# Kernel optimization log

Measured on AMD Instinct MI355X. Metric: run time of the kernel, lower is better.

The kernel has to match this reference:

```python
import jax, jax.numpy as jnp
import numpy as np

N_NODES = 10000
N_EDGES = 320000


def _graph_conv(x, W, b, src, dst, n):
    # DGL GraphConv, norm='both': D_out^{-1/2} on src side, aggregate, D_in^{-1/2} on dst side,
    # then linear + bias. Degrees clamped at 1 (allow_zero_in_degree=True).
    ones = jnp.ones(src.shape[0], dtype=x.dtype)
    deg_out = jnp.clip(jax.ops.segment_sum(ones, src, num_segments=n), 1.0)
    deg_in = jnp.clip(jax.ops.segment_sum(ones, dst, num_segments=n), 1.0)
    h = x * jax.lax.rsqrt(deg_out)[:, None]          # [n, f] scaled source feats
    agg = jax.ops.segment_sum(h[src], dst, num_segments=n)  # gather + scatter-add
    agg = agg * jax.lax.rsqrt(deg_in)[:, None]
    return agg @ W + b


def setup_inputs() -> dict:
    key = jax.random.key(0)
    ks = jax.random.split(key, 8)
    in_dim, h1, h2 = 512, 256, 128
    features = jax.random.normal(ks[0], (N_NODES, in_dim), dtype=jnp.float32)
    src = jax.random.randint(ks[1], (N_EDGES,), 0, N_NODES)
    dst = jax.random.randint(ks[2], (N_EDGES,), 0, N_NODES)
    noise = jax.random.normal(ks[3], (N_NODES, h2), dtype=jnp.float32)
    W1 = jax.random.normal(ks[4], (in_dim, h1), dtype=jnp.float32) / np.sqrt(in_dim)
    b1 = jnp.zeros((h1,), dtype=jnp.float32)
    W2 = jax.random.normal(ks[5], (h1, h2), dtype=jnp.float32) / np.sqrt(h1)
    b2 = jnp.zeros((h2,), dtype=jnp.float32)
    W3 = jax.random.normal(ks[6], (h1, h2), dtype=jnp.float32) / np.sqrt(h1)
    b3 = jnp.zeros((h2,), dtype=jnp.float32)
    return {"features": features, "src": src, "dst": dst, "noise": noise,
            "W1": W1, "b1": b1, "W2": W2, "b2": b2, "W3": W3, "b3": b3}


def reference(features, src, dst, noise, W1, b1, W2, b2, W3, b3):
    n = features.shape[0]
    h = jax.nn.relu(_graph_conv(features, W1, b1, src, dst, n))
    mean = _graph_conv(h, W2, b2, src, dst, n)
    log_std = _graph_conv(h, W3, b3, src, dst, n)
    z = mean + noise * jnp.exp(log_std)              # reparameterization
    adj_rec = jax.nn.sigmoid(z @ z.T)                # inner-product decoder [N, N]
    return adj_rec
```

## Files before the change

kernel.cpp:

```cpp
#include <hip/hip_runtime.h>
#include <hip/hip_fp16.h>


#define NN 10000
#define NE 320000
#define FD 512
#define H1 256
#define H2 128

typedef _Float16 half8 __attribute__((ext_vector_type(8)));
typedef _Float16 half4 __attribute__((ext_vector_type(4)));
typedef float f32x4 __attribute__((ext_vector_type(4)));

__global__ void k_zero3(int* __restrict__ a, int* __restrict__ b, int* __restrict__ c, int n) {
    int i = blockIdx.x * blockDim.x + threadIdx.x;
    if (i < n) { a[i] = 0; b[i] = 0; c[i] = 0; }
}

__global__ void k_count(const int* __restrict__ src, const int* __restrict__ dst,
                        int* __restrict__ co, int* __restrict__ ci) {
    int e = blockIdx.x * blockDim.x + threadIdx.x;
    if (e < NE) {
        atomicAdd(&co[src[e]], 1);
        atomicAdd(&ci[dst[e]], 1);
    }
}

__global__ __launch_bounds__(1024) void k_scan(const int* __restrict__ ci, const int* __restrict__ co,
                                               int* __restrict__ row_ptr,
                                               float* __restrict__ rs_in, float* __restrict__ rs_out) {
    __shared__ int sm[1024];
    int tid = threadIdx.x;
    const int CH = (NN + 1023) / 1024;
    int base = tid * CH;
    int local[CH];
    int s = 0;
    #pragma unroll
    for (int i = 0; i < CH; ++i) {
        int idx = base + i;
        local[i] = s;
        if (idx < NN) s += ci[idx];
    }
    sm[tid] = s;
    __syncthreads();
    for (int off = 1; off < 1024; off <<= 1) {
        int v = (tid >= off) ? sm[tid - off] : 0;
        __syncthreads();
        sm[tid] += v;
        __syncthreads();
    }
    int excl = sm[tid] - s;
    #pragma unroll
    for (int i = 0; i < CH; ++i) {
        int idx = base + i;
        if (idx < NN) row_ptr[idx] = excl + local[i];
    }
    if (tid == 1023) row_ptr[NN] = sm[1023];
    for (int i = tid; i < NN; i += 1024) {
        int a = ci[i], b = co[i];
        rs_in[i]  = rsqrtf((float)(a > 1 ? a : 1));
        rs_out[i] = rsqrtf((float)(b > 1 ? b : 1));
    }
}

__global__ void k_bucket(const int* __restrict__ src, const int* __restrict__ dst,
                         const int* __restrict__ row_ptr, int* __restrict__ cursor,
                         int* __restrict__ esrc) {
    int e = blockIdx.x * blockDim.x + threadIdx.x;
    if (e < NE) {
        int d = dst[e];
        int p = row_ptr[d] + atomicAdd(&cursor[d], 1);
        esrc[p] = src[e];
    }
}

__global__ void k_castW(const float* __restrict__ W1, const float* __restrict__ W2,
                        const float* __restrict__ W3,
                        _Float16* __restrict__ W1Th, _Float16* __restrict__ W1Tl,
                        _Float16* __restrict__ WcTh, _Float16* __restrict__ WcTl) {
    int idx = blockIdx.x * blockDim.x + threadIdx.x;
    if (idx < FD * H1) {
        int k = idx >> 8, n = idx & 255;
        float v = W1[idx];
        _Float16 h = (_Float16)v;
        W1Th[n * FD + k] = h;
        W1Tl[n * FD + k] = (_Float16)(v - (float)h);
    } else if (idx < FD * H1 + H1 * H1) {
        int j = idx - FD * H1;
        int k = j >> 8, n = j & 255;
        float v = (n < H2) ? W2[k * H2 + n] : W3[k * H2 + (n - H2)];
        _Float16 h = (_Float16)v;
        WcTh[n * H1 + k] = h;
        WcTl[n * H1 + k] = (_Float16)(v - (float)h);
    }
}

__global__ __launch_bounds__(256) void k_gemm1(
    const float* __restrict__ A, const float* __restrict__ ascale,
    const _Float16* __restrict__ BTh, const _Float16* __restrict__ BTl,
    _Float16* __restrict__ C, int M) {
    const int K = FD;
    __shared__ __align__(16) _Float16 Ahs[64][72];
    __shared__ __align__(16) _Float16 Als[64][72];
    __shared__ __align__(16) _Float16 Bhs[64][72];
    __shared__ __align__(16) _Float16 Bls[64][72];
    int tid = threadIdx.x;
    int lane = tid & 63;
    int w = tid >> 6;
    int wr = (w >> 1) * 32, wc = (w & 1) * 32;
    int bm = blockIdx.x * 64, bn = blockIdx.y * 64;
    f32x4 acc[2][2] = {};
    for (int k0 = 0; k0 < K; k0 += 64) {
        __syncthreads();
        #pragma unroll
        for (int i = 0; i < 4; ++i) {
            int lin = i * 256 + tid;
            int r = lin >> 4, c = lin & 15;
            int gr = bm + r;
            float4 v = {0.f, 0.f, 0.f, 0.f};
            float s = 1.0f;
            if (gr < M) {
                v = *(const float4*)(A + (size_t)gr * K + k0 + c * 4);
                s = ascale[gr];
            }
            v.x *= s; v.y *= s; v.z *= s; v.w *= s;
            half4 hh = { (_Float16)v.x, (_Float16)v.y, (_Float16)v.z, (_Float16)v.w };
            half4 ll = { (_Float16)(v.x - (float)hh[0]), (_Float16)(v.y - (float)hh[1]),
                         (_Float16)(v.z - (float)hh[2]), (_Float16)(v.w - (float)hh[3]) };
            *(half4*)&Ahs[r][c * 4] = hh;
            *(half4*)&Als[r][c * 4] = ll;
        }
        #pragma unroll
        for (int i = 0; i < 2; ++i) {
            int lin = i * 256 + tid;
            int r = lin >> 3, c = lin & 7;
            *(int4*)&Bhs[r][c * 8] = *(const int4*)(BTh + (size_t)(bn + r) * K + k0 + c * 8);
            *(int4*)&Bls[r][c * 8] = *(const int4*)(BTl + (size_t)(bn + r) * K + k0 + c * 8);
        }
        __syncthreads();
        #pragma unroll
        for (int ks = 0; ks < 2; ++ks) {
            int kof = ks * 32 + ((lane >> 4) << 3);
            half8 ah[2], al[2], bh[2], bl[2];
            #pragma unroll
            for (int f = 0; f < 2; ++f) {
                ah[f] = *(const half8*)&Ahs[wr + f * 16 + (lane & 15)][kof];
                al[f] = *(const half8*)&Als[wr + f * 16 + (lane & 15)][kof];
                bh[f] = *(const half8*)&Bhs[wc + f * 16 + (lane & 15)][kof];
                bl[f] = *(const half8*)&Bls[wc + f * 16 + (lane & 15)][kof];
            }
            #pragma unroll
            for (int i = 0; i < 2; ++i)
                #pragma unroll
                for (int j = 0; j < 2; ++j) {
                    acc[i][j] = __builtin_amdgcn_mfma_f32_16x16x32_f16(ah[i], bh[j], acc[i][j], 0, 0, 0);
                    acc[i][j] = __builtin_amdgcn_mfma_f32_16x16x32_f16(ah[i], bl[j], acc[i][j], 0, 0, 0);
                    acc[i][j] = __builtin_amdgcn_mfma_f32_16x16x32_f16(al[i], bh[j], acc[i][j], 0, 0, 0);
                }
        }
    }
    int quad = lane >> 4, c16 = lane & 15;
    #pragma unroll
    for (int i = 0; i < 2; ++i) {
        int row0 = bm + wr + i * 16 + quad * 4;
        #pragma unroll
        for (int j = 0; j < 2; ++j) {
            int col = bn + wc + j * 16 + c16;
            #pragma unroll
            for (int r = 0; r < 4; ++r) {
                int row = row0 + r;
                if (row < M) C[(size_t)row * H1 + col] = (_Float16)acc[i][j][r];
            }
        }
    }
}

__global__ __launch_bounds__(256) void k_gemm2z(
    const float* __restrict__ A,
    const _Float16* __restrict__ BTh, const _Float16* __restrict__ BTl,
    const float* __restrict__ b2, const float* __restrict__ b3,
    const float* __restrict__ noise, _Float16* __restrict__ Zh, int M) {
    const int K = H1;
    __shared__ __align__(16) _Float16 Ahs[64][72];
    __shared__ __align__(16) _Float16 Als[64][72];
    __shared__ __align__(16) _Float16 Bmh[64][72];
    __shared__ __align__(16) _Float16 Bml[64][72];
    __shared__ __align__(16) _Float16 Blh[64][72];
    __shared__ __align__(16) _Float16 Bll[64][72];
    int tid = threadIdx.x;
    int lane = tid & 63;
    int w = tid >> 6;
    int wr = (w >> 1) * 32, wc = (w & 1) * 32;
    int bm = blockIdx.x * 64;
    int c0 = blockIdx.y * 64;
    f32x4 accm[2][2] = {};
    f32x4 accl[2][2] = {};
    for (int k0 = 0; k0 < K; k0 += 64) {
        __syncthreads();
        #pragma unroll
        for (int i = 0; i < 4; ++i) {
            int lin = i * 256 + tid;
            int r = lin >> 4, c = lin & 15;
            int gr = bm + r;
            float4 v = {0.f, 0.f, 0.f, 0.f};
            if (gr < M) v = *(const float4*)(A + (size_t)gr * K + k0 + c * 4);
            half4 hh = { (_Float16)v.x, (_Float16)v.y, (_Float16)v.z, (_Float16)v.w };
            half4 ll = { (_Float16)(v.x - (float)hh[0]), (_Float16)(v.y - (float)hh[1]),
                         (_Float16)(v.z - (float)hh[2]), (_Float16)(v.w - (float)hh[3]) };
            *(half4*)&Ahs[r][c * 4] = hh;
            *(half4*)&Als[r][c * 4] = ll;
        }
        #pragma unroll
        for (int i = 0; i < 2; ++i) {
            int lin = i * 256 + tid;
            int r = lin >> 3, c = lin & 7;
            size_t rm = (size_t)(c0 + r) * K + k0 + c * 8;
            size_t rl = (size_t)(128 + c0 + r) * K + k0 + c * 8;
            *(int4*)&Bmh[r][c * 8] = *(const int4*)(BTh + rm);
            *(int4*)&Bml[r][c * 8] = *(const int4*)(BTl + rm);
            *(int4*)&Blh[r][c * 8] = *(const int4*)(BTh + rl);
            *(int4*)&Bll[r][c * 8] = *(const int4*)(BTl + rl);
        }
        __syncthreads();
        #pragma unroll
        for (int ks = 0; ks < 2; ++ks) {
            int kof = ks * 32 + ((lane >> 4) << 3);
            half8 ah[2], al[2], mh[2], ml[2], lh[2], ll[2];
            #pragma unroll
            for (int f = 0; f < 2; ++f) {
                ah[f] = *(const half8*)&Ahs[wr + f * 16 + (lane & 15)][kof];
                al[f] = *(const half8*)&Als[wr + f * 16 + (lane & 15)][kof];
                mh[f] = *(const half8*)&Bmh[wc + f * 16 + (lane & 15)][kof];
                ml[f] = *(const half8*)&Bml[wc + f * 16 + (lane & 15)][kof];
                lh[f] = *(const half8*)&Blh[wc + f * 16 + (lane & 15)][kof];
                ll[f] = *(const half8*)&Bll[wc + f * 16 + (lane & 15)][kof];
            }
            #pragma unroll
            for (int i = 0; i < 2; ++i)
                #pragma unroll
                for (int j = 0; j < 2; ++j) {
                    accm[i][j] = __builtin_amdgcn_mfma_f32_16x16x32_f16(ah[i], mh[j], accm[i][j], 0, 0, 0);
                    accm[i][j] = __builtin_amdgcn_mfma_f32_16x16x32_f16(ah[i], ml[j], accm[i][j], 0, 0, 0);
                    accm[i][j] = __builtin_amdgcn_mfma_f32_16x16x32_f16(al[i], mh[j], accm[i][j], 0, 0, 0);
                    accl[i][j] = __builtin_amdgcn_mfma_f32_16x16x32_f16(ah[i], lh[j], accl[i][j], 0, 0, 0);
                    accl[i][j] = __builtin_amdgcn_mfma_f32_16x16x32_f16(ah[i], ll[j], accl[i][j], 0, 0, 0);
                    accl[i][j] = __builtin_amdgcn_mfma_f32_16x16x32_f16(al[i], lh[j], accl[i][j], 0, 0, 0);
                }
        }
    }
    int quad = lane >> 4, c16 = lane & 15;
    #pragma unroll
    for (int i = 0; i < 2; ++i) {
        int row0 = bm + wr + i * 16 + quad * 4;
        #pragma unroll
        for (int j = 0; j < 2; ++j) {
            int c = c0 + wc + j * 16 + c16;
            float bm_ = b2[c], bl_ = b3[c];
            #pragma unroll
            for (int r = 0; r < 4; ++r) {
                int row = row0 + r;
                if (row < M) {
                    float mean = accm[i][j][r] + bm_;
                    float lsv  = accl[i][j][r] + bl_;
                    float z = mean + noise[(size_t)row * H2 + c] * __expf(lsv);
                    Zh[(size_t)row * H2 + c] = (_Float16)z;
                }
            }
        }
    }
}

template <bool FIRST>
__global__ __launch_bounds__(256) void k_agg(const _Float16* __restrict__ in,
                                             _Float16* __restrict__ outh, float* __restrict__ outf,
                                             const int* __restrict__ esrc, const int* __restrict__ row_ptr,
                                             const float* __restrict__ rs_in, const float* __restrict__ rs_out,
                                             const float* __restrict__ bias) {
    int node = (blockIdx.x * blockDim.x + threadIdx.x) >> 6;
    int lane = threadIdx.x & 63;
    if (node >= NN) return;
    int beg = row_ptr[node], end = row_ptr[node + 1];
    float a0 = 0.f, a1 = 0.f, a2 = 0.f, a3 = 0.f;
    int e = beg;
    for (; e + 4 <= end; e += 4) {
        int s0 = esrc[e + 0], s1 = esrc[e + 1], s2 = esrc[e + 2], s3 = esrc[e + 3];
        half4 v0 = ((const half4*)(in + (size_t)s0 * H1))[lane];
        half4 v1 = ((const half4*)(in + (size_t)s1 * H1))[lane];
        half4 v2 = ((const half4*)(in + (size_t)s2 * H1))[lane];
        half4 v3 = ((const half4*)(in + (size_t)s3 * H1))[lane];
        a0 += (float)v0[0] + (float)v1[0] + (float)v2[0] + (float)v3[0];
        a1 += (float)v0[1] + (float)v1[1] + (float)v2[1] + (float)v3[1];
        a2 += (float)v0[2] + (float)v1[2] + (float)v2[2] + (float)v3[2];
        a3 += (float)v0[3] + (float)v1[3] + (float)v2[3] + (float)v3[3];
    }
    for (; e < end; ++e) {
        half4 v0 = ((const half4*)(in + (size_t)esrc[e] * H1))[lane];
        a0 += (float)v0[0]; a1 += (float)v0[1]; a2 += (float)v0[2]; a3 += (float)v0[3];
    }
    float si = rs_in[node];
    a0 *= si; a1 *= si; a2 *= si; a3 *= si;
    if (FIRST) {
        float4 bb = ((const float4*)bias)[lane];
        float so = rs_out[node];
        a0 = fmaxf(a0 + bb.x, 0.f) * so;
        a1 = fmaxf(a1 + bb.y, 0.f) * so;
        a2 = fmaxf(a2 + bb.z, 0.f) * so;
        a3 = fmaxf(a3 + bb.w, 0.f) * so;
        half4 hh = { (_Float16)a0, (_Float16)a1, (_Float16)a2, (_Float16)a3 };
        ((half4*)(outh + (size_t)node * H1))[lane] = hh;
    } else {
        float4 r = { a0, a1, a2, a3 };
        ((float4*)(outf + (size_t)node * H1))[lane] = r;
    }
}

__global__ __launch_bounds__(256) void k_decoder(const _Float16* __restrict__ Z, float* __restrict__ out) {
    __shared__ __align__(16) _Float16 As[128][72];
    __shared__ __align__(16) _Float16 Bs[128][72];
    int tid = threadIdx.x;
    int lane = tid & 63;
    int w = tid >> 6;
    int wrow = (w >> 1) * 64;
    int wcol = (w & 1) * 64;
    int rowBase = blockIdx.y * 128;
    int colBase = blockIdx.x * 128;
    f32x4 acc[4][4] = {};
    for (int s = 0; s < 2; ++s) {
        __syncthreads();
        #pragma unroll
        for (int i = 0; i < 4; ++i) {
            int lin = i * 256 + tid;
            int r = lin >> 3, c = lin & 7;
            int4 v = {0, 0, 0, 0};
            int gr = rowBase + r;
            if (gr < NN) v = *(const int4*)(Z + (size_t)gr * H2 + s * 64 + c * 8);
            *(int4*)&As[r][c * 8] = v;
            int4 u = {0, 0, 0, 0};
            int gc = colBase + r;
            if (gc < NN) u = *(const int4*)(Z + (size_t)gc * H2 + s * 64 + c * 8);
            *(int4*)&Bs[r][c * 8] = u;
        }
        __syncthreads();
        #pragma unroll
        for (int kk = 0; kk < 2; ++kk) {
            int kof = kk * 32 + ((lane >> 4) << 3);
            half8 a[4], b[4];
            #pragma unroll
            for (int f = 0; f < 4; ++f) a[f] = *(const half8*)&As[wrow + f * 16 + (lane & 15)][kof];
            #pragma unroll
            for (int f = 0; f < 4; ++f) b[f] = *(const half8*)&Bs[wcol + f * 16 + (lane & 15)][kof];
            #pragma unroll
            for (int i = 0; i < 4; ++i)
                #pragma unroll
                for (int j = 0; j < 4; ++j)
                    acc[i][j] = __builtin_amdgcn_mfma_f32_16x16x32_f16(a[i], b[j], acc[i][j], 0, 0, 0);
        }
    }
    #pragma unroll
    for (int i = 0; i < 4; ++i) {
        int row0 = rowBase + wrow + i * 16 + ((lane >> 4) << 2);
        #pragma unroll
        for (int j = 0; j < 4; ++j) {
            int col = colBase + wcol + j * 16 + (lane & 15);
            if (col < NN) {
                #pragma unroll
                for (int r = 0; r < 4; ++r) {
                    int row = row0 + r;
                    if (row < NN) {
                        float x = acc[i][j][r];
                        float sg = __builtin_amdgcn_rcpf(1.0f + __expf(-x));
                        __builtin_nontemporal_store(sg, out + (size_t)row * NN + col);
                    }
                }
            }
        }
    }
}

extern "C" void kernel_launch(void* const* d_in, const int* in_sizes, int n_in,
                              void* d_out, int out_size, void* d_ws, size_t ws_size,
                              hipStream_t stream) {
    const float* features = (const float*)d_in[0];
    const int*   src      = (const int*)d_in[1];
    const int*   dst      = (const int*)d_in[2];
    const float* noise    = (const float*)d_in[3];
    const float* W1 = (const float*)d_in[4];
    const float* b1 = (const float*)d_in[5];
    const float* W2 = (const float*)d_in[6];
    const float* b2 = (const float*)d_in[7];
    const float* W3 = (const float*)d_in[8];
    const float* b3 = (const float*)d_in[9];
    float* out = (float*)d_out;
    (void)in_sizes; (void)n_in; (void)out_size; (void)ws_size;

    char* ws = (char*)d_ws;
    size_t off = 0;
    auto alloc = [&](size_t bytes) -> void* {
        void* p = ws + off;
        off += (bytes + 255) & ~(size_t)255;
        return p;
    };
    int* degc_out = (int*)alloc(NN * sizeof(int));
    int* degc_in  = (int*)alloc(NN * sizeof(int));
    int* row_ptr  = (int*)alloc((NN + 1) * sizeof(int));
    int* cursor   = (int*)alloc(NN * sizeof(int));
    int* esrc     = (int*)alloc(NE * sizeof(int));
    float* rs_out = (float*)alloc(NN * sizeof(float));
    float* rs_in  = (float*)alloc(NN * sizeof(float));
    _Float16* W1Th = (_Float16*)alloc((size_t)H1 * FD * sizeof(_Float16));
    _Float16* W1Tl = (_Float16*)alloc((size_t)H1 * FD * sizeof(_Float16));
    _Float16* WcTh = (_Float16*)alloc((size_t)H1 * H1 * sizeof(_Float16));
    _Float16* WcTl = (_Float16*)alloc((size_t)H1 * H1 * sizeof(_Float16));
    _Float16* y1h  = (_Float16*)alloc((size_t)NN * H1 * sizeof(_Float16));
    _Float16* hh   = (_Float16*)alloc((size_t)NN * H1 * sizeof(_Float16));
    float* agg2    = (float*)alloc((size_t)NN * H1 * sizeof(float));
    _Float16* Zh   = (_Float16*)alloc((size_t)NN * H2 * sizeof(_Float16));

    k_zero3<<<(NN + 255) / 256, 256, 0, stream>>>(degc_out, degc_in, cursor, NN);
    k_count<<<(NE + 255) / 256, 256, 0, stream>>>(src, dst, degc_out, degc_in);
    k_scan<<<1, 1024, 0, stream>>>(degc_in, degc_out, row_ptr, rs_in, rs_out);
    k_bucket<<<(NE + 255) / 256, 256, 0, stream>>>(src, dst, row_ptr, cursor, esrc);
    k_castW<<<(FD * H1 + H1 * H1 + 255) / 256, 256, 0, stream>>>(
        W1, W2, W3, W1Th, W1Tl, WcTh, WcTl);

    k_gemm1<<<dim3((NN + 63) / 64, H1 / 64), 256, 0, stream>>>(
        features, rs_out, W1Th, W1Tl, y1h, NN);
    k_agg<true><<<NN / 4, 256, 0, stream>>>(y1h, hh, nullptr, esrc, row_ptr, rs_in, rs_out, b1);
    k_agg<false><<<NN / 4, 256, 0, stream>>>(hh, nullptr, agg2, esrc, row_ptr, rs_in, nullptr, nullptr);
    k_gemm2z<<<dim3((NN + 63) / 64, H2 / 64), 256, 0, stream>>>(
        agg2, WcTh, WcTl, b2, b3, noise, Zh, NN);
    k_decoder<<<dim3((NN + 127) / 128, (NN + 127) / 128), 256, 0, stream>>>(Zh, out);
}
```

Baseline: 625.6 us.

## Exploit decoder symmetry, reorder layer-2 GEMM before aggregation, widen aggregation gathers

The decoder now launches only the upper-triangular 128x128 tiles and writes each off-diagonal tile twice, once directly and once transposed, so the Z·Zᵀ matmul work is roughly halved. The layer-2 linear transform is applied before aggregation, so the second aggregation gathers fp16 rows and fuses the bias, exp and noise epilogue, removing the fp32 agg2 buffer and the split-precision A operand. The aggregation kernel uses half-wave splits with 16-byte gathers. In exchange, the transposed writes are strided 16-byte stores rather than coalesced nontemporal ones, and the aggregated intermediate is now held in fp16, which may cost some accuracy.

Result: no change. 634.9 us (+1.5%).

```diff
diff --git a/kernel.cpp b/kernel.cpp
--- a/kernel.cpp
+++ b/kernel.cpp
@@ -175,76 +175,50 @@
     }
 }
 
-__global__ __launch_bounds__(256) void k_gemm2z(
-    const float* __restrict__ A,
+__global__ __launch_bounds__(256) void k_gemm2(
+    const _Float16* __restrict__ A,
     const _Float16* __restrict__ BTh, const _Float16* __restrict__ BTl,
-    const float* __restrict__ b2, const float* __restrict__ b3,
-    const float* __restrict__ noise, _Float16* __restrict__ Zh, int M) {
+    _Float16* __restrict__ C, int M) {
     const int K = H1;
     __shared__ __align__(16) _Float16 Ahs[64][72];
-    __shared__ __align__(16) _Float16 Als[64][72];
-    __shared__ __align__(16) _Float16 Bmh[64][72];
-    __shared__ __align__(16) _Float16 Bml[64][72];
-    __shared__ __align__(16) _Float16 Blh[64][72];
-    __shared__ __align__(16) _Float16 Bll[64][72];
+    __shared__ __align__(16) _Float16 Bhs[64][72];
+    __shared__ __align__(16) _Float16 Bls[64][72];
     int tid = threadIdx.x;
     int lane = tid & 63;
     int w = tid >> 6;
     int wr = (w >> 1) * 32, wc = (w & 1) * 32;
-    int bm = blockIdx.x * 64;
-    int c0 = blockIdx.y * 64;
-    f32x4 accm[2][2] = {};
-    f32x4 accl[2][2] = {};
+    int bm = blockIdx.x * 64, bn = blockIdx.y * 64;
+    f32x4 acc[2][2] = {};
     for (int k0 = 0; k0 < K; k0 += 64) {
         __syncthreads();
-        #pragma unroll
-        for (int i = 0; i < 4; ++i) {
-            int lin = i * 256 + tid;
-            int r = lin >> 4, c = lin & 15;
-            int gr = bm + r;
-            float4 v = {0.f, 0.f, 0.f, 0.f};
-            if (gr < M) v = *(const float4*)(A + (size_t)gr * K + k0 + c * 4);
-            half4 hh = { (_Float16)v.x, (_Float16)v.y, (_Float16)v.z, (_Float16)v.w };
-            half4 ll = { (_Float16)(v.x - (float)hh[0]), (_Float16)(v.y - (float)hh[1]),
-                         (_Float16)(v.z - (float)hh[2]), (_Float16)(v.w - (float)hh[3]) };
-            *(half4*)&Ahs[r][c * 4] = hh;
-            *(half4*)&Als[r][c * 4] = ll;
-        }
         #pragma unroll
         for (int i = 0; i < 2; ++i) {
             int lin = i * 256 + tid;
             int r = lin >> 3, c = lin & 7;
-            size_t rm = (size_t)(c0 + r) * K + k0 + c * 8;
-            size_t rl = (size_t)(128 + c0 + r) * K + k0 + c * 8;
-            *(int4*)&Bmh[r][c * 8] = *(const int4*)(BTh + rm);
-            *(int4*)&Bml[r][c * 8] = *(const int4*)(BTl + rm);
-            *(int4*)&Blh[r][c * 8] = *(const int4*)(BTh + rl);
-            *(int4*)&Bll[r][c * 8] = *(const int4*)(BTl + rl);
+            int gr = bm + r;
+            int4 va = {0, 0, 0, 0};
+            if (gr < M) va = *(const int4*)(A + (size_t)gr * K + k0 + c * 8);
+            *(int4*)&Ahs[r][c * 8] = va;
+            *(int4*)&Bhs[r][c * 8] = *(const int4*)(BTh + (size_t)(bn + r) * K + k0 + c * 8);
+            *(int4*)&Bls[r][c * 8] = *(const int4*)(BTl + (size_t)(bn + r) * K + k0 + c * 8);
         }
         __syncthreads();
         #pragma unroll
         for (int ks = 0; ks < 2; ++ks) {
             int kof = ks * 32 + ((lane >> 4) << 3);
-            half8 ah[2], al[2], mh[2], ml[2], lh[2], ll[2];
+            half8 ah[2], bh[2], bl[2];
             #pragma unroll
             for (int f = 0; f < 2; ++f) {
                 ah[f] = *(const half8*)&Ahs[wr + f * 16 + (lane & 15)][kof];
-                al[f] = *(const half8*)&Als[wr + f * 16 + (lane & 15)][kof];
-                mh[f] = *(const half8*)&Bmh[wc + f * 16 + (lane & 15)][kof];
-                ml[f] = *(const half8*)&Bml[wc + f * 16 + (lane & 15)][kof];
-                lh[f] = *(const half8*)&Blh[wc + f * 16 + (lane & 15)][kof];
-                ll[f] = *(const half8*)&Bll[wc + f * 16 + (lane & 15)][kof];
+                bh[f] = *(const half8*)&Bhs[wc + f * 16 + (lane & 15)][kof];
+                bl[f] = *(const half8*)&Bls[wc + f * 16 + (lane & 15)][kof];
             }
             #pragma unroll
             for (int i = 0; i < 2; ++i)
                 #pragma unroll
                 for (int j = 0; j < 2; ++j) {
-                    accm[i][j] = __builtin_amdgcn_mfma_f32_16x16x32_f16(ah[i], mh[j], accm[i][j], 0, 0, 0);
-                    accm[i][j] = __builtin_amdgcn_mfma_f32_16x16x32_f16(ah[i], ml[j], accm[i][j], 0, 0, 0);
-                    accm[i][j] = __builtin_amdgcn_mfma_f32_16x16x32_f16(al[i], mh[j], accm[i][j], 0, 0, 0);
-                    accl[i][j] = __builtin_amdgcn_mfma_f32_16x16x32_f16(ah[i], lh[j], accl[i][j], 0, 0, 0);
-                    accl[i][j] = __builtin_amdgcn_mfma_f32_16x16x32_f16(ah[i], ll[j], accl[i][j], 0, 0, 0);
-                    accl[i][j] = __builtin_amdgcn_mfma_f32_16x16x32_f16(al[i], lh[j], accl[i][j], 0, 0, 0);
+                    acc[i][j] = __builtin_amdgcn_mfma_f32_16x16x32_f16(ah[i], bh[j], acc[i][j], 0, 0, 0);
+                    acc[i][j] = __builtin_amdgcn_mfma_f32_16x16x32_f16(ah[i], bl[j], acc[i][j], 0, 0, 0);
                 }
         }
     }
@@ -254,17 +228,11 @@
         int row0 = bm + wr + i * 16 + quad * 4;
         #pragma unroll
         for (int j = 0; j < 2; ++j) {
-            int c = c0 + wc + j * 16 + c16;
-            float bm_ = b2[c], bl_ = b3[c];
+            int col = bn + wc + j * 16 + c16;
             #pragma unroll
             for (int r = 0; r < 4; ++r) {
                 int row = row0 + r;
-                if (row < M) {
-                    float mean = accm[i][j][r] + bm_;
-                    float lsv  = accl[i][j][r] + bl_;
-                    float z = mean + noise[(size_t)row * H2 + c] * __expf(lsv);
-                    Zh[(size_t)row * H2 + c] = (_Float16)z;
-                }
+                if (row < M) C[(size_t)row * H1 + col] = (_Float16)acc[i][j][r];
             }
         }
     }
@@ -272,58 +240,98 @@
 
 template <bool FIRST>
 __global__ __launch_bounds__(256) void k_agg(const _Float16* __restrict__ in,
-                                             _Float16* __restrict__ outh, float* __restrict__ outf,
+                                             _Float16* __restrict__ outh,
                                              const int* __restrict__ esrc, const int* __restrict__ row_ptr,
                                              const float* __restrict__ rs_in, const float* __restrict__ rs_out,
-                                             const float* __restrict__ bias) {
-    int node = (blockIdx.x * blockDim.x + threadIdx.x) >> 6;
+                                             const float* __restrict__ b1,
+                                             const float* __restrict__ b2, const float* __restrict__ b3,
+                                             const float* __restrict__ noise) {
+    int wid = (blockIdx.x * blockDim.x + threadIdx.x) >> 6;
     int lane = threadIdx.x & 63;
-    if (node >= NN) return;
-    int beg = row_ptr[node], end = row_ptr[node + 1];
-    float a0 = 0.f, a1 = 0.f, a2 = 0.f, a3 = 0.f;
-    int e = beg;
-    for (; e + 4 <= end; e += 4) {
-        int s0 = esrc[e + 0], s1 = esrc[e + 1], s2 = esrc[e + 2], s3 = esrc[e + 3];
-        half4 v0 = ((const half4*)(in + (size_t)s0 * H1))[lane];
-        half4 v1 = ((const half4*)(in + (size_t)s1 * H1))[lane];
-        half4 v2 = ((const half4*)(in + (size_t)s2 * H1))[lane];
-        half4 v3 = ((const half4*)(in + (size_t)s3 * H1))[lane];
-        a0 += (float)v0[0] + (float)v1[0] + (float)v2[0] + (float)v3[0];
-        a1 += (float)v0[1] + (float)v1[1] + (float)v2[1] + (float)v3[1];
-        a2 += (float)v0[2] + (float)v1[2] + (float)v2[2] + (float)v3[2];
-        a3 += (float)v0[3] + (float)v1[3] + (float)v2[3] + (float)v3[3];
-    }
-    for (; e < end; ++e) {
-        half4 v0 = ((const half4*)(in + (size_t)esrc[e] * H1))[lane];
-        a0 += (float)v0[0]; a1 += (float)v0[1]; a2 += (float)v0[2]; a3 += (float)v0[3];
-    }
-    float si = rs_in[node];
-    a0 *= si; a1 *= si; a2 *= si; a3 *= si;
+    if (wid >= NN) return;
+    int sub = lane >> 5, cl = lane & 31;
+    int beg = row_ptr[wid], end = row_ptr[wid + 1];
+    float a[8] = {};
+    const _Float16* basep = in + cl * 8;
+    int e = beg + sub;
+    for (; e + 6 < end; e += 8) {
+        int s0 = esrc[e], s1 = esrc[e + 2], s2 = esrc[e + 4], s3 = esrc[e + 6];
+        half8 v0 = *(const half8*)(basep + (size_t)s0 * H1);
+        half8 v1 = *(const half8*)(basep + (size_t)s1 * H1);
+        half8 v2 = *(const half8*)(basep + (size_t)s2 * H1);
+        half8 v3 = *(const half8*)(basep + (size_t)s3 * H1);
+        #pragma unroll
+        for (int j = 0; j < 8; ++j)
+            a[j] += ((float)v0[j] + (float)v1[j]) + ((float)v2[j] + (float)v3[j]);
+    }
+    for (; e < end; e += 2) {
+        half8 v = *(const half8*)(basep + (size_t)esrc[e] * H1);
+        #pragma unroll
+        for (int j = 0; j < 8; ++j) a[j] += (float)v[j];
+    }
+    #pragma unroll
+    for (int j = 0; j < 8; ++j) a[j] += __shfl_xor(a[j], 32);
+    float si = rs_in[wid];
     if (FIRST) {
-        float4 bb = ((const float4*)bias)[lane];
-        float so = rs_out[node];
-        a0 = fmaxf(a0 + bb.x, 0.f) * so;
-        a1 = fmaxf(a1 + bb.y, 0.f) * so;
-        a2 = fmaxf(a2 + bb.z, 0.f) * so;
-        a3 = fmaxf(a3 + bb.w, 0.f) * so;
-        half4 hh = { (_Float16)a0, (_Float16)a1, (_Float16)a2, (_Float16)a3 };
-        ((half4*)(outh + (size_t)node * H1))[lane] = hh;
+        if (sub == 0) {
+            float so = rs_out[wid];
+            float4 bb0 = *(const float4*)(b1 + cl * 8);
+            float4 bb1 = *(const float4*)(b1 + cl * 8 + 4);
+            float bb[8] = {bb0.x, bb0.y, bb0.z, bb0.w, bb1.x, bb1.y, bb1.z, bb1.w};
+            half8 hh;
+            #pragma unroll
+            for (int j = 0; j < 8; ++j)
+                hh[j] = (_Float16)(fmaxf(a[j] * si + bb[j], 0.f) * so);
+            *(half8*)(outh + (size_t)wid * H1 + cl * 8) = hh;
+        }
     } else {
-        float4 r = { a0, a1, a2, a3 };
-        ((float4*)(outf + (size_t)node * H1))[lane] = r;
+        float ls[8];
+        #pragma unroll
+        for (int j = 0; j < 8; ++j) ls[j] = __shfl_xor(a[j], 16);
+        if (sub == 0 && cl < 16) {
+            int c0 = cl * 8;
+            float4 m0 = *(const float4*)(b2 + c0);
+            float4 m1 = *(const float4*)(b2 + c0 + 4);
+            float4 l0 = *(const float4*)(b3 + c0);
+            float4 l1 = *(const float4*)(b3 + c0 + 4);
+            float bm_[8] = {m0.x, m0.y, m0.z, m0.w, m1.x, m1.y, m1.z, m1.w};
+            float bl_[8] = {l0.x, l0.y, l0.z, l0.w, l1.x, l1.y, l1.z, l1.w};
+            float4 n0 = *(const float4*)(noise + (size_t)wid * H2 + c0);
+            float4 n1 = *(const float4*)(noise + (size_t)wid * H2 + c0 + 4);
+            float nn_[8] = {n0.x, n0.y, n0.z, n0.w, n1.x, n1.y, n1.z, n1.w};
+            half8 zz;
+            #pragma unroll
+            for (int j = 0; j < 8; ++j) {
+                float mean = a[j] * si + bm_[j];
+                float lsv  = ls[j] * si + bl_[j];
+                zz[j] = (_Float16)(mean + nn_[j] * __expf(lsv));
+            }
+            *(half8*)(outh + (size_t)wid * H2 + c0) = zz;
+        }
     }
 }
 
 __global__ __launch_bounds__(256) void k_decoder(const _Float16* __restrict__ Z, float* __restrict__ out) {
+    const int NB = (NN + 127) / 128;
     __shared__ __align__(16) _Float16 As[128][72];
     __shared__ __align__(16) _Float16 Bs[128][72];
+    int t = blockIdx.x;
+    int bi = 0;
+    int startNext = NB;
+    while (startNext <= t) {
+        ++bi;
+        startNext += NB - bi;
+    }
+    int startBi = startNext - (NB - bi);
+    int bj = bi + (t - startBi);
+    int rowBase = bi * 128;
+    int colBase = bj * 128;
+    bool diag = (bi == bj);
     int tid = threadIdx.x;
     int lane = tid & 63;
     int w = tid >> 6;
     int wrow = (w >> 1) * 64;
     int wcol = (w & 1) * 64;
-    int rowBase = blockIdx.y * 128;
-    int colBase = blockIdx.x * 128;
     f32x4 acc[4][4] = {};
     for (int s = 0; s < 2; ++s) {
         __syncthreads();
@@ -362,15 +370,17 @@
         #pragma unroll
         for (int j = 0; j < 4; ++j) {
             int col = colBase + wcol + j * 16 + (lane & 15);
-            if (col < NN) {
+            if (col < NN && row0 < NN) {
+                float sg[4];
                 #pragma unroll
-                for (int r = 0; r < 4; ++r) {
-                    int row = row0 + r;
-                    if (row < NN) {
-                        float x = acc[i][j][r];
-                        float sg = __builtin_amdgcn_rcpf(1.0f + __expf(-x));
-                        __builtin_nontemporal_store(sg, out + (size_t)row * NN + col);
-                    }
+                for (int r = 0; r < 4; ++r)
+                    sg[r] = __builtin_amdgcn_rcpf(1.0f + __expf(-acc[i][j][r]));
+                #pragma unroll
+                for (int r = 0; r < 4; ++r)
+                    __builtin_nontemporal_store(sg[r], out + (size_t)(row0 + r) * NN + col);
+                if (!diag) {
+                    f32x4 v = {sg[0], sg[1], sg[2], sg[3]};
+                    *(f32x4*)(out + (size_t)col * NN + row0) = v;
                 }
             }
         }
@@ -413,7 +423,7 @@
     _Float16* WcTl = (_Float16*)alloc((size_t)H1 * H1 * sizeof(_Float16));
     _Float16* y1h  = (_Float16*)alloc((size_t)NN * H1 * sizeof(_Float16));
     _Float16* hh   = (_Float16*)alloc((size_t)NN * H1 * sizeof(_Float16));
-    float* agg2    = (float*)alloc((size_t)NN * H1 * sizeof(float));
+    _Float16* hw   = (_Float16*)alloc((size_t)NN * H1 * sizeof(_Float16));
     _Float16* Zh   = (_Float16*)alloc((size_t)NN * H2 * sizeof(_Float16));
 
     k_zero3<<<(NN + 255) / 256, 256, 0, stream>>>(degc_out, degc_in, cursor, NN);
@@ -425,9 +435,11 @@
 
     k_gemm1<<<dim3((NN + 63) / 64, H1 / 64), 256, 0, stream>>>(
         features, rs_out, W1Th, W1Tl, y1h, NN);
-    k_agg<true><<<NN / 4, 256, 0, stream>>>(y1h, hh, nullptr, esrc, row_ptr, rs_in, rs_out, b1);
-    k_agg<false><<<NN / 4, 256, 0, stream>>>(hh, nullptr, agg2, esrc, row_ptr, rs_in, nullptr, nullptr);
-    k_gemm2z<<<dim3((NN + 63) / 64, H2 / 64), 256, 0, stream>>>(
-        agg2, WcTh, WcTl, b2, b3, noise, Zh, NN);
-    k_decoder<<<dim3((NN + 127) / 128, (NN + 127) / 128), 256, 0, stream>>>(Zh, out);
-}
+    k_agg<true><<<NN / 4, 256, 0, stream>>>(y1h, hh, esrc, row_ptr, rs_in, rs_out,
+                                            b1, nullptr, nullptr, nullptr);
+    k_gemm2<<<dim3((NN + 63) / 64, H1 / 64), 256, 0, stream>>>(hh, WcTh, WcTl, hw, NN);
+    k_agg<false><<<NN / 4, 256, 0, stream>>>(hw, Zh, esrc, row_ptr, rs_in, nullptr,
+                                             nullptr, b2, b3, noise);
+    const int NB = (NN + 127) / 128;
+    k_decoder<<<NB * (NB + 1) / 2, 256, 0, stream>>>(Zh, out);
+}
```
